# Performance work log

Hardware: AMD Instinct MI355X
Metric: run time of the kernel (lower is better)

Reference implementation:

```python
import jax, jax.numpy as jnp
import numpy as np

N, E, F_IN, F_HID, F_OUT = 50000, 800000, 128, 128, 64


def setup_inputs() -> dict:
    key = jax.random.key(0)
    k_x, k_e, k_w1, k_w2 = jax.random.split(key, 4)
    x = jax.random.normal(k_x, (N, F_IN), dtype=jnp.float32)
    edge_index = jax.random.randint(k_e, (2, E), 0, N, dtype=jnp.int32)
    # GCNConv params (glorot-ish scale)
    W1 = jax.random.normal(k_w1, (F_IN, F_HID), dtype=jnp.float32) * (1.0 / np.sqrt(F_IN))
    b1 = jnp.zeros((F_HID,), dtype=jnp.float32)
    W2 = jax.random.normal(k_w2, (F_HID, F_OUT), dtype=jnp.float32) * (1.0 / np.sqrt(F_HID))
    b2 = jnp.zeros((F_OUT,), dtype=jnp.float32)
    return {"x": x, "edge_index": edge_index, "W1": W1, "b1": b1, "W2": W2, "b2": b2}


def reference(x, edge_index, W1, b1, W2, b2):
    n = x.shape[0]
    # PyG GCNConv: add self-loops, symmetric normalization deg^-1/2 * deg^-1/2
    loops = jnp.arange(n, dtype=edge_index.dtype)
    src = jnp.concatenate([edge_index[0], loops])  # (E+N,)
    dst = jnp.concatenate([edge_index[1], loops])  # (E+N,)
    deg = jax.ops.segment_sum(jnp.ones_like(dst, dtype=x.dtype), dst, num_segments=n)
    dinv = jnp.where(deg > 0, jax.lax.rsqrt(jnp.maximum(deg, 1.0)), 0.0)
    norm = dinv[src] * dinv[dst]  # (E+N,)

    def conv(h, W, b):
        h = h @ W                               # (n, f_out)
        msg = h[src] * norm[:, None]            # gather + scale, (E+N, f_out)
        return jax.ops.segment_sum(msg, dst, num_segments=n) + b

    h = jax.nn.relu(conv(x, W1, b1))  # dropout p=0.0 -> identity
    return conv(h, W2, b2)
```

## Files before the change

### kernel.cpp

```cpp
#include <hip/hip_runtime.h>

typedef __bf16 bf16x8 __attribute__((ext_vector_type(8)));
typedef float  f32x4  __attribute__((ext_vector_type(4)));
typedef int    i32x4  __attribute__((ext_vector_type(4)));
typedef unsigned int u32x4 __attribute__((ext_vector_type(4)));

#define NTLOAD(p)    __builtin_nontemporal_load(p)

__device__ __forceinline__ float bf2f(unsigned short h) {
    return __uint_as_float(((unsigned int)h) << 16);
}
__device__ __forceinline__ unsigned short f2bf(float f) {
    unsigned int u = __float_as_uint(f);
    u += 0x7FFFu + ((u >> 16) & 1u);
    return (unsigned short)(u >> 16);
}
__device__ __forceinline__ void unpack8(u32x4 u, float* v) {
#pragma unroll
    for (int k = 0; k < 4; ++k) {
        v[2 * k]     = __uint_as_float(u[k] << 16);
        v[2 * k + 1] = __uint_as_float(u[k] & 0xFFFF0000u);
    }
}

__device__ __forceinline__ int detect_cnt(const unsigned short* __restrict__ x,
                                          int* sc, int t) {
    int c = 0;
    for (int i = t; i < 4096; i += 256) {
        unsigned e = (x[i] >> 7) & 0xFFu;
        if (e >= 0x88u) ++c;
    }
    sc[t] = c;
    __syncthreads();
    for (int d = 128; d > 0; d >>= 1) {
        if (t < d) sc[t] += sc[t + d];
        __syncthreads();
    }
    return sc[0];
}

template <int COLS>
__device__ __forceinline__ void prepack_one(const void* W, unsigned short* Wp, int idx,
                                            bool isf32) {
    if (idx >= (COLS / 16) * 4 * 64) return;
    int lane = idx & 63;
    int ks   = (idx >> 6) & 3;
    int nt   = idx >> 8;
    int col  = nt * 16 + (lane & 15);
    int krow = ks * 32 + (lane >> 4) * 8;
    unsigned short tmp[8];
#pragma unroll
    for (int j = 0; j < 8; ++j) {
        size_t e = (size_t)(krow + j) * COLS + col;
        float v = isf32 ? ((const float*)W)[e] : bf2f(((const unsigned short*)W)[e]);
        tmp[j] = f2bf(v);
    }
    *(u32x4*)(Wp + (size_t)idx * 8) = *(u32x4*)tmp;
}

__device__ __forceinline__ void partitionA(int pb, const int* __restrict__ src,
                                           const int* __restrict__ dst, int E, int part,
                                           int capg, long long* __restrict__ bedge,
                                           int* __restrict__ bcur) {
    __shared__ int lcnt[8], lpref[9], gbase[8], lcur[8];
    __shared__ long long lbuf[1024];
    int t = threadIdx.x;
    if (t < 8) lcnt[t] = 0;
    __syncthreads();
    int e0 = pb * 1024;
    int g_[4]; long long es_[4]; bool val_[4];
#pragma unroll
    for (int r = 0; r < 4; ++r) {
        int e = e0 + r * 256 + t;
        val_[r] = (e < E);
        int d = val_[r] ? dst[e] : 0;
        int s = val_[r] ? src[e] : 0;
        es_[r] = ((long long)d << 32) | (unsigned)s;
        g_[r] = (int)((unsigned)d / (unsigned)part);
        if (val_[r]) atomicAdd(&lcnt[g_[r]], 1);
    }
    __syncthreads();
    if (t == 0) {
        int run = 0;
#pragma unroll
        for (int g = 0; g < 8; ++g) { lpref[g] = run; run += lcnt[g]; }
        lpref[8] = run;
    }
    __syncthreads();
    if (t < 8) { lcur[t] = lpref[t]; gbase[t] = atomicAdd(&bcur[t], lcnt[t]); }
    __syncthreads();
#pragma unroll
    for (int r = 0; r < 4; ++r) {
        if (val_[r]) {
            int p = atomicAdd(&lcur[g_[r]], 1);
            lbuf[p] = es_[r];
        }
    }
    __syncthreads();
    int total = lpref[8];
    for (int i = t; i < total; i += 256) {
        long long es = lbuf[i];
        int d = (int)(es >> 32);
        int g = (int)((unsigned)d / (unsigned)part);
        int pos = gbase[g] + (i - lpref[g]);
        bedge[(size_t)g * capg + pos] = es;
    }
}

__global__ void k0_prep(const unsigned short* __restrict__ x, int* __restrict__ dflag,
                        int* __restrict__ cnt, int N,
                        const int* __restrict__ src, const int* __restrict__ dst, int E,
                        int part, int capg, long long* __restrict__ bedge,
                        int* __restrict__ bcur, int ZB,
                        const void* __restrict__ W1, const void* __restrict__ W2,
                        const void* __restrict__ b1, const void* __restrict__ b2,
                        unsigned short* __restrict__ Wp1, unsigned short* __restrict__ Wp2,
                        float* __restrict__ b1f, float* __restrict__ b2f) {
    __shared__ int sc[256];
    int t = threadIdx.x;
    int bid = (int)blockIdx.x;
    if (bid < 13) {
        int c = detect_cnt(x, sc, t);
        bool isf32 = (c >= 16);
        if (bid < 8) {
            prepack_one<128>(W1, Wp1, bid * 256 + t, isf32);
        } else if (bid < 12) {
            prepack_one<64>(W2, Wp2, (bid - 8) * 256 + t, isf32);
        } else {
            if (t == 0) dflag[0] = c;
            if (t < 128) b1f[t] = isf32 ? ((const float*)b1)[t]
                                        : bf2f(((const unsigned short*)b1)[t]);
            else if (t < 192) b2f[t - 128] = isf32 ? ((const float*)b2)[t - 128]
                                                   : bf2f(((const unsigned short*)b2)[t - 128]);
        }
    } else if (bid < 13 + ZB) {
        int i = (bid - 13) * 1024 + t * 4;
        if (i + 4 <= N) *(i32x4*)(cnt + i) = (i32x4){0, 0, 0, 0};
        else for (int k = i; k < N; ++k) cnt[k] = 0;
    } else {
        partitionA(bid - 13 - ZB, src, dst, E, part, capg, bedge, bcur);
    }
}

__device__ __forceinline__ void gemm1_body(const void* __restrict__ X,
                                           const unsigned short* __restrict__ Wp,
                                           unsigned short* __restrict__ O, int nstrips,
                                           bool xf32, int blockI,
                                           unsigned short* __restrict__ Ls) {
    constexpr int NT = 8;
    const int wave = threadIdx.x >> 6;
    const int lane = threadIdx.x & 63;
    const int strip = blockI * 4 + wave;
    const bool active = (strip < nstrips);
    const int m = lane & 15;
    const int q = lane >> 4;
    unsigned short* lw = Ls + wave * (16 * 136);

    if (active) {
        const unsigned rowoff = (unsigned)(strip * 16 + m) * 128u + (unsigned)(q * 8);
        f32x4 acc[NT];
#pragma unroll
        for (int nt = 0; nt < NT; ++nt) acc[nt] = (f32x4){0.f, 0.f, 0.f, 0.f};

#pragma unroll
        for (int ks = 0; ks < 4; ++ks) {
            bf16x8 a;
            if (xf32) {
                const float* xp = (const float*)X + rowoff + ks * 32;
                f32x4 u = *(const f32x4*)xp;
                f32x4 v = *((const f32x4*)xp + 1);
                unsigned short tmp[8];
                tmp[0] = f2bf(u[0]); tmp[1] = f2bf(u[1]);
                tmp[2] = f2bf(u[2]); tmp[3] = f2bf(u[3]);
                tmp[4] = f2bf(v[0]); tmp[5] = f2bf(v[1]);
                tmp[6] = f2bf(v[2]); tmp[7] = f2bf(v[3]);
                a = *(bf16x8*)tmp;
            } else {
                a = *(const bf16x8*)((const unsigned short*)X + rowoff + ks * 32);
            }
#pragma unroll
            for (int nt = 0; nt < NT; ++nt) {
                bf16x8 b = *(const bf16x8*)(Wp + (unsigned)(((nt * 4 + ks) * 64 + lane) * 8));
                acc[nt] = __builtin_amdgcn_mfma_f32_16x16x32_bf16(a, b, acc[nt], 0, 0, 0);
            }
        }

#pragma unroll
        for (int nt = 0; nt < NT; ++nt) {
#pragma unroll
            for (int r = 0; r < 4; ++r)
                lw[(q * 4 + r) * 136 + nt * 16 + m] = f2bf(acc[nt][r]);
        }
    }

    __syncthreads();

    if (active) {
        const int r0 = strip * 16;
#pragma unroll
        for (int i = 0; i < 4; ++i) {
            int c = lane + 64 * i;
            int row = c >> 4, k = c & 15;
            u32x4 v = *(const u32x4*)&lw[row * 136 + k * 8];
            *(u32x4*)(O + (unsigned)(r0 + row) * 128u + (unsigned)(k * 8)) = v;
        }
    }
}

__global__ __launch_bounds__(256) void k1_scatter_gemm1(
        const long long* __restrict__ bedge, const int* __restrict__ bcur,
        int* __restrict__ cnt, int* __restrict__ adj, int capg, int SB,
        const void* __restrict__ X, const unsigned short* __restrict__ Wp1,
        unsigned short* __restrict__ Hb, int nstrips, const int* __restrict__ dflag) {
    __shared__ unsigned short Ls[4 * 16 * 136];
    if ((int)blockIdx.x < SB) {
        int sb = (int)blockIdx.x;
        int g = sb & 7;
        int ib = sb >> 3;
        int M = min(bcur[g], capg);
        const long long* bp = bedge + (size_t)g * capg;
        int base = ib * 2048;
        if (base >= M) return;
#pragma unroll
        for (int k = 0; k < 8; ++k) {
            int e = base + k * 256 + (int)threadIdx.x;
            if (e < M) {
                long long ev = NTLOAD(bp + e);
                int s = (int)(unsigned)(ev & 0xFFFFFFFFll);
                int d = (int)(ev >> 32);
                int p = atomicAdd(&cnt[d], 1);
                if (p < 64) adj[((unsigned)d << 6) + p] = s;
            }
        }
    } else {
        gemm1_body(X, Wp1, Hb, nstrips, (*dflag >= 16), blockIdx.x - SB, Ls);
    }
}

__global__ void k2_dinv(const int* __restrict__ cnt, float* __restrict__ dinv, int N) {
    int i = blockIdx.x * 1024 + threadIdx.x * 4;
    if (i + 4 <= N) {
        i32x4 c = *(const i32x4*)(cnt + i);
        f32x4 d;
#pragma unroll
        for (int k = 0; k < 4; ++k) d[k] = rsqrtf((float)c[k] + 1.0f);
        *(f32x4*)(dinv + i) = d;
    } else {
        for (int k = i; k < N; ++k) dinv[k] = rsqrtf((float)cnt[k] + 1.0f);
    }
}

__global__ __launch_bounds__(256) void gather1_gemm2(
        const unsigned short* __restrict__ Hb, const float* __restrict__ dinv,
        const int* __restrict__ cnt, const float* __restrict__ b,
        const int* __restrict__ adj, const unsigned short* __restrict__ Wp2,
        unsigned short* __restrict__ H2b, int N) {
    __shared__ unsigned short Rs[16][136];
    __shared__ unsigned short Hs[16][72];
    const int strip = blockIdx.x;
    const int tid = threadIdx.x;
    const int lane = tid & 63;

    {
        int ndl = tid >> 4;
        int nd = strip * 16 + ndl;
        int l15 = lane & 15;
        int gbase = lane & ~15;
        unsigned f8 = (unsigned)(l15 * 8);
        if (nd < N) {
            float acc[8];
#pragma unroll
            for (int k = 0; k < 8; ++k) acc[k] = 0.f;
            int len = min(cnt[nd], 64);
            const int* arow = adj + ((unsigned)nd << 6);
            for (int c = 0; c < len; c += 16) {
                int rem = len - c;
                int myadj = (l15 < rem) ? NTLOAD((int*)&arow[c + l15]) : 0;
                float myw = (l15 < rem) ? dinv[myadj] : 0.f;
#pragma unroll
                for (int t = 0; t < 16; t += 8) {
                    if (t >= rem) break;
                    int sI[8];
#pragma unroll
                    for (int k = 0; k < 8; ++k) sI[k] = __shfl(myadj, gbase + t + k, 64);
                    u32x4 u[8];
#pragma unroll
                    for (int k = 0; k < 8; ++k)
                        u[k] = *(const u32x4*)(Hb + ((unsigned)sI[k] << 7) + f8);
                    float n[8];
#pragma unroll
                    for (int k = 0; k < 8; ++k) n[k] = __shfl(myw, gbase + t + k, 64);
#pragma unroll
                    for (int k = 0; k < 8; ++k) {
                        float v[8];
                        unpack8(u[k], v);
#pragma unroll
                        for (int j = 0; j < 8; ++j) acc[j] = fmaf(v[j], n[k], acc[j]);
                    }
                }
            }
            float dd = dinv[nd];
            float hv[8], bb[8];
            unpack8(*(const u32x4*)(Hb + ((unsigned)nd << 7) + f8), hv);
            *(f32x4*)&bb[0] = *(const f32x4*)(b + f8);
            *(f32x4*)&bb[4] = *(const f32x4*)(b + f8 + 4);
            unsigned short o[8];
#pragma unroll
            for (int k = 0; k < 8; ++k) {
                float a = fmaf(fmaf(hv[k], dd, acc[k]), dd, bb[k]);
                o[k] = f2bf(fmaxf(a, 0.f));
            }
            *(u32x4*)&Rs[ndl][f8] = *(u32x4*)o;
        } else {
            *(u32x4*)&Rs[ndl][f8] = (u32x4){0u, 0u, 0u, 0u};
        }
    }
    __syncthreads();

    {
        const int nt = tid >> 6;
        const int m = lane & 15;
        const int q = lane >> 4;
        f32x4 acc = (f32x4){0.f, 0.f, 0.f, 0.f};
#pragma unroll
        for (int ks = 0; ks < 4; ++ks) {
            bf16x8 a = *(const bf16x8*)&Rs[m][ks * 32 + q * 8];
            bf16x8 bfr = *(const bf16x8*)(Wp2 + (unsigned)(((nt * 4 + ks) * 64 + lane) * 8));
            acc = __builtin_amdgcn_mfma_f32_16x16x32_bf16(a, bfr, acc, 0, 0, 0);
        }
        const int rr = strip * 16 + q * 4;
        f32x4 dv;
        if (rr + 3 < N) {
            dv = *(const f32x4*)(dinv + rr);
        } else {
#pragma unroll
            for (int r = 0; r < 4; ++r) dv[r] = (rr + r < N) ? dinv[rr + r] : 0.f;
        }
#pragma unroll
        for (int r = 0; r < 4; ++r)
            Hs[q * 4 + r][nt * 16 + m] = f2bf(acc[r] * dv[r]);
    }
    __syncthreads();
    if (tid < 128) {
        int row = tid >> 3, k = tid & 7;
        int grow = strip * 16 + row;
        if (grow < N) {
            u32x4 v = *(const u32x4*)&Hs[row][k * 8];
            *(u32x4*)(H2b + (unsigned)grow * 64u + (unsigned)(k * 8)) = v;
        }
    }
}

__global__ void gather2(const unsigned short* __restrict__ H2b, const float* __restrict__ dinv,
                        const int* __restrict__ cnt, const float* __restrict__ b,
                        const int* __restrict__ adj, void* __restrict__ out,
                        int N, const int* __restrict__ dflag) {
    bool isf32 = (*dflag >= 16);
    int nd = blockIdx.x * 32 + (threadIdx.x >> 3);
    int lane = threadIdx.x & 63;
    int l7 = lane & 7;
    int gbase = lane & ~7;
    unsigned f8 = (unsigned)(l7 * 8);
    if (nd >= N) return;

    float acc[8];
#pragma unroll
    for (int k = 0; k < 8; ++k) acc[k] = 0.f;

    int len = min(cnt[nd], 64);
    const int* arow = adj + ((unsigned)nd << 6);
    for (int c = 0; c < len; c += 8) {
        int rem = len - c;
        int myadj = (l7 < rem) ? NTLOAD((int*)&arow[c + l7]) : 0;
        int sI[8];
#pragma unroll
        for (int k = 0; k < 8; ++k) sI[k] = __shfl(myadj, gbase + k, 64);
        u32x4 u[8];
#pragma unroll
        for (int k = 0; k < 8; ++k)
            u[k] = *(const u32x4*)(H2b + ((unsigned)sI[k] << 6) + f8);
        float n[8];
#pragma unroll
        for (int k = 0; k < 8; ++k) n[k] = (k < rem) ? 1.f : 0.f;
#pragma unroll
        for (int k = 0; k < 8; ++k) {
            float v[8];
            unpack8(u[k], v);
#pragma unroll
            for (int j = 0; j < 8; ++j) acc[j] = fmaf(v[j], n[k], acc[j]);
        }
    }
    float dd = dinv[nd];
    float hv[8], bb[8];
    unpack8(*(const u32x4*)(H2b + ((unsigned)nd << 6) + f8), hv);
    *(f32x4*)&bb[0] = *(const f32x4*)(b + f8);
    *(f32x4*)&bb[4] = *(const f32x4*)(b + f8 + 4);
    float r[8];
#pragma unroll
    for (int k = 0; k < 8; ++k) r[k] = fmaf(acc[k] + hv[k], dd, bb[k]);
    if (isf32) {
        float* op = (float*)out + (unsigned)nd * 64u + f8;
        *(f32x4*)op       = *(f32x4*)&r[0];
        *(f32x4*)(op + 4) = *(f32x4*)&r[4];
    } else {
        unsigned short o[8];
#pragma unroll
        for (int k = 0; k < 8; ++k) o[k] = f2bf(r[k]);
        *(u32x4*)((unsigned short*)out + (unsigned)nd * 64u + f8) = *(u32x4*)o;
    }
}

extern "C" void kernel_launch(void* const* d_in, const int* in_sizes, int n_in,
                              void* d_out, int out_size, void* d_ws, size_t ws_size,
                              hipStream_t stream) {
    const void* x  = d_in[0];
    const int*  ei = (const int*)d_in[1];
    const void* W1 = d_in[2];
    const void* b1 = d_in[3];
    const void* W2 = d_in[4];
    const void* b2 = d_in[5];

    const int N = in_sizes[0] / 128;
    const int E = in_sizes[1] / 2;
    const int* src = ei;
    const int* dst = ei + E;

    float* ws = (float*)d_ws;
    size_t off = 0;
    auto alloc = [&](size_t n) { size_t p = off; off += (n + 15) & ~(size_t)15; return p; };
    int*   dflag  = (int*)(ws + alloc(64));
    int*   bcur   = (int*)(ws + alloc(64));
    int*   cnt    = (int*)(ws + alloc(N));
    float* dinv   = ws + alloc(N);
    int*   adj    = (int*)(ws + alloc((size_t)N * 64));
    const int capg = (E >> 3) + 16384;
    long long* bedge = (long long*)(ws + alloc((size_t)capg * 8 * 2));
    unsigned short* Hb  = (unsigned short*)(ws + alloc((size_t)N * 64));
    unsigned short* Wp1 = (unsigned short*)(ws + alloc(8192));
    unsigned short* Wp2 = (unsigned short*)(ws + alloc(4096));
    float* b1f    = ws + alloc(128);
    float* b2f    = ws + alloc(64);
    unsigned short* H2b = (unsigned short*)(ws + alloc((size_t)N * 32));

    const int part = (N + 7) >> 3;
    const int ZB   = (N + 1023) / 1024;
    const int PB   = (E + 1023) / 1024;
    const int SB   = 8 * ((capg + 2047) / 2048);
    const int nstrips = (N + 15) / 16;
    const int GB = (nstrips + 3) / 4;
    const int NB32 = (N + 31) / 32;

    hipMemsetAsync(bcur, 0, 64, stream);
    k0_prep<<<13 + ZB + PB, 256, 0, stream>>>((const unsigned short*)x, dflag, cnt, N,
                                              src, dst, E, part, capg, bedge, bcur, ZB,
                                              W1, W2, b1, b2, Wp1, Wp2, b1f, b2f);
    k1_scatter_gemm1<<<SB + GB, 256, 0, stream>>>(bedge, bcur, cnt, adj, capg, SB,
                                                  x, Wp1, Hb, nstrips, dflag);
    k2_dinv<<<ZB, 256, 0, stream>>>(cnt, dinv, N);
    gather1_gemm2<<<nstrips, 256, 0, stream>>>(Hb, dinv, cnt, b1f, adj, Wp2, H2b, N);
    gather2<<<NB32, 256, 0, stream>>>(H2b, dinv, cnt, b2f, adj, d_out, N, dflag);
}
```

Measured before the change: 185.0 us.

## Merge GEMM1 into prep kernel, drop dinv kernel, recompute rsqrt inline

```diff
diff --git a/kernel.cpp b/kernel.cpp
--- a/kernel.cpp
+++ b/kernel.cpp
@@ -61,9 +61,12 @@
 __device__ __forceinline__ void partitionA(int pb, const int* __restrict__ src,
                                            const int* __restrict__ dst, int E, int part,
                                            int capg, long long* __restrict__ bedge,
-                                           int* __restrict__ bcur) {
-    __shared__ int lcnt[8], lpref[9], gbase[8], lcur[8];
-    __shared__ long long lbuf[1024];
+                                           int* __restrict__ bcur, char* sm) {
+    int* lcnt  = (int*)sm;
+    int* lpref = lcnt + 8;
+    int* gbs   = lpref + 9;
+    int* lcur  = gbs + 8;
+    long long* lbuf = (long long*)(sm + 512);
     int t = threadIdx.x;
     if (t < 8) lcnt[t] = 0;
     __syncthreads();
@@ -87,7 +90,7 @@
         lpref[8] = run;
     }
     __syncthreads();
-    if (t < 8) { lcur[t] = lpref[t]; gbase[t] = atomicAdd(&bcur[t], lcnt[t]); }
+    if (t < 8) { lcur[t] = lpref[t]; gbs[t] = atomicAdd(&bcur[t], lcnt[t]); }
     __syncthreads();
 #pragma unroll
     for (int r = 0; r < 4; ++r) {
@@ -102,51 +105,16 @@
         long long es = lbuf[i];
         int d = (int)(es >> 32);
         int g = (int)((unsigned)d / (unsigned)part);
-        int pos = gbase[g] + (i - lpref[g]);
+        int pos = gbs[g] + (i - lpref[g]);
         bedge[(size_t)g * capg + pos] = es;
     }
 }
 
-__global__ void k0_prep(const unsigned short* __restrict__ x, int* __restrict__ dflag,
-                        int* __restrict__ cnt, int N,
-                        const int* __restrict__ src, const int* __restrict__ dst, int E,
-                        int part, int capg, long long* __restrict__ bedge,
-                        int* __restrict__ bcur, int ZB,
-                        const void* __restrict__ W1, const void* __restrict__ W2,
-                        const void* __restrict__ b1, const void* __restrict__ b2,
-                        unsigned short* __restrict__ Wp1, unsigned short* __restrict__ Wp2,
-                        float* __restrict__ b1f, float* __restrict__ b2f) {
-    __shared__ int sc[256];
-    int t = threadIdx.x;
-    int bid = (int)blockIdx.x;
-    if (bid < 13) {
-        int c = detect_cnt(x, sc, t);
-        bool isf32 = (c >= 16);
-        if (bid < 8) {
-            prepack_one<128>(W1, Wp1, bid * 256 + t, isf32);
-        } else if (bid < 12) {
-            prepack_one<64>(W2, Wp2, (bid - 8) * 256 + t, isf32);
-        } else {
-            if (t == 0) dflag[0] = c;
-            if (t < 128) b1f[t] = isf32 ? ((const float*)b1)[t]
-                                        : bf2f(((const unsigned short*)b1)[t]);
-            else if (t < 192) b2f[t - 128] = isf32 ? ((const float*)b2)[t - 128]
-                                                   : bf2f(((const unsigned short*)b2)[t - 128]);
-        }
-    } else if (bid < 13 + ZB) {
-        int i = (bid - 13) * 1024 + t * 4;
-        if (i + 4 <= N) *(i32x4*)(cnt + i) = (i32x4){0, 0, 0, 0};
-        else for (int k = i; k < N; ++k) cnt[k] = 0;
-    } else {
-        partitionA(bid - 13 - ZB, src, dst, E, part, capg, bedge, bcur);
-    }
-}
-
-__device__ __forceinline__ void gemm1_body(const void* __restrict__ X,
-                                           const unsigned short* __restrict__ Wp,
-                                           unsigned short* __restrict__ O, int nstrips,
-                                           bool xf32, int blockI,
-                                           unsigned short* __restrict__ Ls) {
+__device__ __forceinline__ void gemm1_body_lds(const void* __restrict__ X,
+                                               const unsigned short* __restrict__ Wl,
+                                               unsigned short* __restrict__ O, int nstrips,
+                                               bool xf32, int blockI,
+                                               unsigned short* __restrict__ Ls) {
     constexpr int NT = 8;
     const int wave = threadIdx.x >> 6;
     const int lane = threadIdx.x & 63;
@@ -180,7 +148,7 @@
             }
 #pragma unroll
             for (int nt = 0; nt < NT; ++nt) {
-                bf16x8 b = *(const bf16x8*)(Wp + (unsigned)(((nt * 4 + ks) * 64 + lane) * 8));
+                bf16x8 b = *(const bf16x8*)(Wl + (unsigned)(((nt * 4 + ks) * 64 + lane) * 8));
                 acc[nt] = __builtin_amdgcn_mfma_f32_16x16x32_bf16(a, b, acc[nt], 0, 0, 0);
             }
         }
@@ -207,53 +175,104 @@
     }
 }
 
-__global__ __launch_bounds__(256) void k1_scatter_gemm1(
+__global__ __launch_bounds__(256) void k0_mega(
+        const unsigned short* __restrict__ x, int* __restrict__ dflag,
+        int* __restrict__ cnt, int N,
+        const int* __restrict__ src, const int* __restrict__ dst, int E,
+        int part, int capg, long long* __restrict__ bedge, int* __restrict__ bcur,
+        const void* __restrict__ W1, const void* __restrict__ W2,
+        const void* __restrict__ b1, const void* __restrict__ b2,
+        unsigned short* __restrict__ Wp2, float* __restrict__ b1f, float* __restrict__ b2f,
+        unsigned short* __restrict__ Hb, int nstrips, int GB, int PB, int ZB) {
+    __shared__ __attribute__((aligned(16))) char sm[1024 + 32768 + 17408];
+    int t = threadIdx.x;
+    int bid = (int)blockIdx.x;
+    int mn = min(GB, PB);
+    int nInter = 2 * mn;
+    int role, idx;
+    if (bid < nInter) { role = bid & 1; idx = bid >> 1; }
+    else {
+        int r = bid - nInter;
+        int extra = (GB > PB) ? GB - PB : PB - GB;
+        if (r < extra) { role = (GB > PB) ? 0 : 1; idx = mn + r; }
+        else {
+            r -= extra;
+            if (r < ZB) { role = 2; idx = r; }
+            else        { role = 3; idx = r - ZB; }
+        }
+    }
+
+    if (role == 0) {
+        int* sc = (int*)sm;
+        int c = detect_cnt(x, sc, t);
+        bool xf32 = (c >= 16);
+        unsigned short* Wl = (unsigned short*)(sm + 1024);
+        const float* W1f = (const float*)W1;
+        const unsigned short* W1h = (const unsigned short*)W1;
+        for (int i = t; i < 2048; i += 256) {
+            int lane = i & 63, ks = (i >> 6) & 3, nt = i >> 8;
+            int col = nt * 16 + (lane & 15);
+            int krow = ks * 32 + (lane >> 4) * 8;
+            unsigned short tmp[8];
+#pragma unroll
+            for (int j = 0; j < 8; ++j) {
+                int e = (krow + j) * 128 + col;
+                float v = xf32 ? W1f[e] : bf2f(W1h[e]);
+                tmp[j] = f2bf(v);
+            }
+            *(u32x4*)(Wl + (unsigned)i * 8) = *(u32x4*)tmp;
+        }
+        __syncthreads();
+        gemm1_body_lds(x, Wl, Hb, nstrips, xf32, idx,
+                       (unsigned short*)(sm + 1024 + 32768));
+    } else if (role == 1) {
+        partitionA(idx, src, dst, E, part, capg, bedge, bcur, sm);
+    } else if (role == 2) {
+        int i = idx * 1024 + t * 4;
+        if (i + 4 <= N) *(i32x4*)(cnt + i) = (i32x4){0, 0, 0, 0};
+        else for (int k = i; k < N; ++k) cnt[k] = 0;
+    } else {
+        int* sc = (int*)sm;
+        int c = detect_cnt(x, sc, t);
+        bool isf32 = (c >= 16);
+        if (idx < 4) {
+            prepack_one<64>(W2, Wp2, idx * 256 + t, isf32);
+        } else {
+            if (t == 0) dflag[0] = c;
+            if (t < 128) b1f[t] = isf32 ? ((const float*)b1)[t]
+                                        : bf2f(((const unsigned short*)b1)[t]);
+            else if (t < 192) b2f[t - 128] = isf32 ? ((const float*)b2)[t - 128]
+                                                   : bf2f(((const unsigned short*)b2)[t - 128]);
+        }
+    }
+}
+
+__global__ __launch_bounds__(256) void k1_scatter(
         const long long* __restrict__ bedge, const int* __restrict__ bcur,
-        int* __restrict__ cnt, int* __restrict__ adj, int capg, int SB,
-        const void* __restrict__ X, const unsigned short* __restrict__ Wp1,
-        unsigned short* __restrict__ Hb, int nstrips, const int* __restrict__ dflag) {
-    __shared__ unsigned short Ls[4 * 16 * 136];
-    if ((int)blockIdx.x < SB) {
-        int sb = (int)blockIdx.x;
-        int g = sb & 7;
-        int ib = sb >> 3;
-        int M = min(bcur[g], capg);
-        const long long* bp = bedge + (size_t)g * capg;
-        int base = ib * 2048;
-        if (base >= M) return;
-#pragma unroll
-        for (int k = 0; k < 8; ++k) {
-            int e = base + k * 256 + (int)threadIdx.x;
-            if (e < M) {
-                long long ev = NTLOAD(bp + e);
-                int s = (int)(unsigned)(ev & 0xFFFFFFFFll);
-                int d = (int)(ev >> 32);
-                int p = atomicAdd(&cnt[d], 1);
-                if (p < 64) adj[((unsigned)d << 6) + p] = s;
-            }
-        }
-    } else {
-        gemm1_body(X, Wp1, Hb, nstrips, (*dflag >= 16), blockIdx.x - SB, Ls);
-    }
-}
-
-__global__ void k2_dinv(const int* __restrict__ cnt, float* __restrict__ dinv, int N) {
-    int i = blockIdx.x * 1024 + threadIdx.x * 4;
-    if (i + 4 <= N) {
-        i32x4 c = *(const i32x4*)(cnt + i);
-        f32x4 d;
-#pragma unroll
-        for (int k = 0; k < 4; ++k) d[k] = rsqrtf((float)c[k] + 1.0f);
-        *(f32x4*)(dinv + i) = d;
-    } else {
-        for (int k = i; k < N; ++k) dinv[k] = rsqrtf((float)cnt[k] + 1.0f);
+        int* __restrict__ cnt, int* __restrict__ adj, int capg) {
+    int g = (int)blockIdx.x & 7;
+    int ib = (int)blockIdx.x >> 3;
+    int M = min(bcur[g], capg);
+    const long long* bp = bedge + (size_t)g * capg;
+    int base = ib * 1024;
+    if (base >= M) return;
+#pragma unroll
+    for (int k = 0; k < 4; ++k) {
+        int e = base + k * 256 + (int)threadIdx.x;
+        if (e < M) {
+            long long ev = NTLOAD(bp + e);
+            int s = (int)(unsigned)(ev & 0xFFFFFFFFll);
+            int d = (int)(ev >> 32);
+            int p = atomicAdd(&cnt[d], 1);
+            if (p < 64) adj[((unsigned)d << 6) + p] = s;
+        }
     }
 }
 
 __global__ __launch_bounds__(256) void gather1_gemm2(
-        const unsigned short* __restrict__ Hb, const float* __restrict__ dinv,
-        const int* __restrict__ cnt, const float* __restrict__ b,
-        const int* __restrict__ adj, const unsigned short* __restrict__ Wp2,
+        const unsigned short* __restrict__ Hb, const int* __restrict__ cnt,
+        const float* __restrict__ b, const int* __restrict__ adj,
+        const unsigned short* __restrict__ Wp2,
         unsigned short* __restrict__ H2b, int N) {
     __shared__ unsigned short Rs[16][136];
     __shared__ unsigned short Hs[16][72];
@@ -276,7 +295,7 @@
             for (int c = 0; c < len; c += 16) {
                 int rem = len - c;
                 int myadj = (l15 < rem) ? NTLOAD((int*)&arow[c + l15]) : 0;
-                float myw = (l15 < rem) ? dinv[myadj] : 0.f;
+                float myw = (l15 < rem) ? rsqrtf((float)cnt[myadj] + 1.0f) : 0.f;
 #pragma unroll
                 for (int t = 0; t < 16; t += 8) {
                     if (t >= rem) break;
@@ -299,7 +318,7 @@
                     }
                 }
             }
-            float dd = dinv[nd];
+            float dd = rsqrtf((float)cnt[nd] + 1.0f);
             float hv[8], bb[8];
             unpack8(*(const u32x4*)(Hb + ((unsigned)nd << 7) + f8), hv);
             *(f32x4*)&bb[0] = *(const f32x4*)(b + f8);
@@ -330,12 +349,9 @@
         }
         const int rr = strip * 16 + q * 4;
         f32x4 dv;
-        if (rr + 3 < N) {
-            dv = *(const f32x4*)(dinv + rr);
-        } else {
-#pragma unroll
-            for (int r = 0; r < 4; ++r) dv[r] = (rr + r < N) ? dinv[rr + r] : 0.f;
-        }
+#pragma unroll
+        for (int r = 0; r < 4; ++r)
+            dv[r] = (rr + r < N) ? rsqrtf((float)cnt[rr + r] + 1.0f) : 0.f;
 #pragma unroll
         for (int r = 0; r < 4; ++r)
             Hs[q * 4 + r][nt * 16 + m] = f2bf(acc[r] * dv[r]);
@@ -351,10 +367,9 @@
     }
 }
 
-__global__ void gather2(const unsigned short* __restrict__ H2b, const float* __restrict__ dinv,
-                        const int* __restrict__ cnt, const float* __restrict__ b,
-                        const int* __restrict__ adj, void* __restrict__ out,
-                        int N, const int* __restrict__ dflag) {
+__global__ void gather2(const unsigned short* __restrict__ H2b, const int* __restrict__ cnt,
+                        const float* __restrict__ b, const int* __restrict__ adj,
+                        void* __restrict__ out, int N, const int* __restrict__ dflag) {
     bool isf32 = (*dflag >= 16);
     int nd = blockIdx.x * 32 + (threadIdx.x >> 3);
     int lane = threadIdx.x & 63;
@@ -390,7 +405,7 @@
             for (int j = 0; j < 8; ++j) acc[j] = fmaf(v[j], n[k], acc[j]);
         }
     }
-    float dd = dinv[nd];
+    float dd = rsqrtf((float)cnt[nd] + 1.0f);
     float hv[8], bb[8];
     unpack8(*(const u32x4*)(H2b + ((unsigned)nd << 6) + f8), hv);
     *(f32x4*)&bb[0] = *(const f32x4*)(b + f8);
@@ -431,12 +446,10 @@
     int*   dflag  = (int*)(ws + alloc(64));
     int*   bcur   = (int*)(ws + alloc(64));
     int*   cnt    = (int*)(ws + alloc(N));
-    float* dinv   = ws + alloc(N);
     int*   adj    = (int*)(ws + alloc((size_t)N * 64));
     const int capg = (E >> 3) + 16384;
     long long* bedge = (long long*)(ws + alloc((size_t)capg * 8 * 2));
     unsigned short* Hb  = (unsigned short*)(ws + alloc((size_t)N * 64));
-    unsigned short* Wp1 = (unsigned short*)(ws + alloc(8192));
     unsigned short* Wp2 = (unsigned short*)(ws + alloc(4096));
     float* b1f    = ws + alloc(128);
     float* b2f    = ws + alloc(64);
@@ -445,18 +458,16 @@
     const int part = (N + 7) >> 3;
     const int ZB   = (N + 1023) / 1024;
     const int PB   = (E + 1023) / 1024;
-    const int SB   = 8 * ((capg + 2047) / 2048);
     const int nstrips = (N + 15) / 16;
     const int GB = (nstrips + 3) / 4;
+    const int SB = 8 * ((capg + 1023) / 1024);
     const int NB32 = (N + 31) / 32;
 
     hipMemsetAsync(bcur, 0, 64, stream);
-    k0_prep<<<13 + ZB + PB, 256, 0, stream>>>((const unsigned short*)x, dflag, cnt, N,
-                                              src, dst, E, part, capg, bedge, bcur, ZB,
-                                              W1, W2, b1, b2, Wp1, Wp2, b1f, b2f);
-    k1_scatter_gemm1<<<SB + GB, 256, 0, stream>>>(bedge, bcur, cnt, adj, capg, SB,
-                                                  x, Wp1, Hb, nstrips, dflag);
-    k2_dinv<<<ZB, 256, 0, stream>>>(cnt, dinv, N);
-    gather1_gemm2<<<nstrips, 256, 0, stream>>>(Hb, dinv, cnt, b1f, adj, Wp2, H2b, N);
-    gather2<<<NB32, 256, 0, stream>>>(H2b, dinv, cnt, b2f, adj, d_out, N, dflag);
-}
+    k0_mega<<<GB + PB + ZB + 5, 256, 0, stream>>>(
+        (const unsigned short*)x, dflag, cnt, N, src, dst, E, part, capg, bedge, bcur,
+        W1, W2, b1, b2, Wp2, b1f, b2f, Hb, nstrips, GB, PB, ZB);
+    k1_scatter<<<SB, 256, 0, stream>>>(bedge, bcur, cnt, adj, capg);
+    gather1_gemm2<<<nstrips, 256, 0, stream>>>(Hb, cnt, b1f, adj, Wp2, H2b, N);
+    gather2<<<NB32, 256, 0, stream>>>(H2b, cnt, b2f, adj, d_out, N, dflag);
+}
```

After: 213.2 us. 15.2% more time.
